# Kernel tuning notes

Measured on AMD Instinct MI355X. Metric: run time of the kernel, lower is better.

## Reference

```python
import jax, jax.numpy as jnp
import numpy as np

B, T, C = 1, 2048, 3072
H, HKV, D = 24, 8, 128          # heads, kv heads, head_dim
G = H // HKV                    # gqa groups = 3
ROPE_BASE = 10000.0


def _rope_cos_sin(seq_len, dim, dtype):
    inv_freq = 1.0 / (ROPE_BASE ** (jnp.arange(0, dim, 2, dtype=jnp.float32) / dim))
    t = jnp.arange(seq_len, dtype=jnp.float32)
    freqs = t[:, None] * inv_freq[None, :]            # [T, D/2]
    emb = jnp.concatenate([freqs, freqs], axis=-1)    # [T, D]
    return jnp.cos(emb).astype(dtype), jnp.sin(emb).astype(dtype)


def _rotate_half(x):
    h = x.shape[-1] // 2
    return jnp.concatenate([-x[..., h:], x[..., :h]], axis=-1)


def setup_inputs() -> dict:
    key = jax.random.key(0)
    ks = jax.random.split(key, 5)
    s = 0.02
    return {
        "x":  jax.random.normal(ks[0], (B, T, C), dtype=jnp.float32),
        "Wq": jax.random.normal(ks[1], (C, H * D), dtype=jnp.float32) * s,
        "Wk": jax.random.normal(ks[2], (C, HKV * D), dtype=jnp.float32) * s,
        "Wv": jax.random.normal(ks[3], (C, HKV * D), dtype=jnp.float32) * s,
        "Wo": jax.random.normal(ks[4], (C, C), dtype=jnp.float32) * s,
    }


def reference(x, Wq, Wk, Wv, Wo):
    b, t, c = x.shape
    # projections -> [B, H(or HKV), T, D]
    q = (x @ Wq).reshape(b, t, H, D).transpose(0, 2, 1, 3)
    k = (x @ Wk).reshape(b, t, HKV, D).transpose(0, 2, 1, 3)
    v = (x @ Wv).reshape(b, t, HKV, D).transpose(0, 2, 1, 3)
    # GQA: repeat_interleave kv heads to full head count
    k = jnp.repeat(k, G, axis=1)
    v = jnp.repeat(v, G, axis=1)
    # RoPE
    cos, sin = _rope_cos_sin(t, D, x.dtype)           # [T, D]
    cos = cos[None, None]                             # [1,1,T,D]
    sin = sin[None, None]
    q = q * cos + _rotate_half(q) * sin
    k = k * cos + _rotate_half(k) * sin
    # causal SDPA
    scale = 1.0 / jnp.sqrt(jnp.asarray(D, dtype=x.dtype))
    scores = jnp.einsum('bhqd,bhkd->bhqk', q, k) * scale
    causal = jnp.tril(jnp.ones((t, t), dtype=bool))
    scores = jnp.where(causal[None, None], scores, jnp.finfo(x.dtype).min)
    attn = jax.nn.softmax(scores, axis=-1)
    out = jnp.einsum('bhqk,bhkd->bhqd', attn, v)      # [B,H,T,D]
    out = out.transpose(0, 2, 1, 3).reshape(b, t, c)
    return out @ Wo
```

## Files before the change

kernel.cpp:

```cpp
#include <hip/hip_runtime.h>
#include <cstdint>

#define T_SEQ 2048
#define C_DIM 3072
#define NH    24
#define NKV   8
#define HD    128

typedef short  bf16x8 __attribute__((ext_vector_type(8)));
typedef float  f32x4  __attribute__((ext_vector_type(4)));

__device__ __forceinline__ ushort f2bf(float f) {
    union { float f; uint32_t u; } v; v.f = f;
    uint32_t r = (v.u + 0x7FFF + ((v.u >> 16) & 1)) >> 16;
    return (ushort)r;
}

__device__ __forceinline__ uint32_t cvtpk_bf16(float lo, float hi) {
    uint32_t r;
    asm("v_cvt_pk_bf16_f32 %0, %1, %2" : "=v"(r) : "v"(lo), "v"(hi));
    return r;
}

__device__ __forceinline__ float fast_exp2(float x) {
#if __has_builtin(__builtin_amdgcn_exp2f)
    return __builtin_amdgcn_exp2f(x);
#else
    return exp2f(x);
#endif
}

__device__ __forceinline__ void gll16(const void* g, void* lds) {
    __builtin_amdgcn_global_load_lds(
        (const __attribute__((address_space(1))) uint32_t*)g,
        (__attribute__((address_space(3))) uint32_t*)lds, 16, 0, 0);
}

__global__ __launch_bounds__(64) void rope_table(float* __restrict__ cosT,
                                                 float* __restrict__ sinT) {
    int t = blockIdx.x;
    int j = threadIdx.x;
    float inv = powf(10000.0f, -(float)j * (1.0f / 64.0f));
    float ang = (float)t * inv;
    cosT[t * 64 + j] = cosf(ang);
    sinT[t * 64 + j] = sinf(ang);
}

__global__ __launch_bounds__(256) void convert_x(const float* __restrict__ x,
                                                 ushort* __restrict__ xb) {
    int i = blockIdx.x * 256 + threadIdx.x;
    int stride = gridDim.x * 256;
    const int n4 = (T_SEQ * C_DIM) / 4;
    for (; i < n4; i += stride) {
        float4 v = ((const float4*)x)[i];
        ushort4 o;
        o.x = f2bf(v.x); o.y = f2bf(v.y); o.z = f2bf(v.z); o.w = f2bf(v.w);
        ((ushort4*)xb)[i] = o;
    }
}

__global__ __launch_bounds__(256) void transpose_w(const float* __restrict__ src,
                                                   ushort* __restrict__ dst,
                                                   int ldN) {
    __shared__ float sT[64][65];
    const int n0 = blockIdx.x * 64;
    const int k0 = blockIdx.y * 64;
    const int r  = threadIdx.x >> 4;
    const int c4 = (threadIdx.x & 15) * 4;
    #pragma unroll
    for (int i = 0; i < 4; ++i) {
        int kk = r + i * 16;
        float4 v = *(const float4*)&src[(size_t)(k0 + kk) * ldN + n0 + c4];
        sT[kk][c4 + 0] = v.x; sT[kk][c4 + 1] = v.y;
        sT[kk][c4 + 2] = v.z; sT[kk][c4 + 3] = v.w;
    }
    __syncthreads();
    #pragma unroll
    for (int i = 0; i < 4; ++i) {
        int nn = r + i * 16;
        ushort4 o;
        o.x = f2bf(sT[c4 + 0][nn]); o.y = f2bf(sT[c4 + 1][nn]);
        o.z = f2bf(sT[c4 + 2][nn]); o.w = f2bf(sT[c4 + 3][nn]);
        *(ushort4*)&dst[(size_t)(n0 + nn) * C_DIM + k0 + c4] = o;
    }
}

__global__ __launch_bounds__(256) void qkv_gemm_mfma(
    const ushort* __restrict__ xb, const ushort* __restrict__ WbT,
    const float* __restrict__ cosT, const float* __restrict__ sinT,
    ushort* __restrict__ Qb, ushort* __restrict__ Kb, ushort* __restrict__ Vt) {

    __shared__ ushort sA[128 * 64];
    __shared__ ushort sB[128 * 64];

    const int bx = blockIdx.x;
    const int by = blockIdx.y;
    const int tid = threadIdx.x;
    const int w = tid >> 6, l = tid & 63, g = l >> 4, c = l & 15;
    const int m0 = by * 128, n0 = bx * 128;

    f32x4 acc[2][8];
    #pragma unroll
    for (int m = 0; m < 2; ++m)
        #pragma unroll
        for (int n = 0; n < 8; ++n) acc[m][n] = {0.f, 0.f, 0.f, 0.f};

    const int ch = (w * 4) * 64 + l;
    for (int k0 = 0; k0 < C_DIM; k0 += 64) {
        __syncthreads();
        #pragma unroll
        for (int u = 0; u < 4; ++u) {
            int chu = ch + u * 64;
            int row = chu >> 3, sub = chu & 7;
            int sc  = sub ^ (row & 7);
            gll16(xb  + (size_t)(m0 + row) * C_DIM + k0 + sc * 8, &sA[(w * 4 + u) * 512]);
            gll16(WbT + (size_t)(n0 + row) * C_DIM + k0 + sc * 8, &sB[(w * 4 + u) * 512]);
        }
        __syncthreads();

        #pragma unroll
        for (int kc = 0; kc < 2; ++kc) {
            bf16x8 a[2], b[8];
            #pragma unroll
            for (int m = 0; m < 2; ++m) {
                int row = w * 32 + m * 16 + c;
                int chp = (kc * 4 + g) ^ (row & 7);
                a[m] = *(const bf16x8*)&sA[row * 64 + chp * 8];
            }
            #pragma unroll
            for (int n = 0; n < 8; ++n) {
                int row = n * 16 + c;
                int chp = (kc * 4 + g) ^ (row & 7);
                b[n] = *(const bf16x8*)&sB[row * 64 + chp * 8];
            }
            #pragma unroll
            for (int m = 0; m < 2; ++m)
                #pragma unroll
                for (int n = 0; n < 8; ++n)
                    acc[m][n] = __builtin_amdgcn_mfma_f32_16x16x32_bf16(a[m], b[n], acc[m][n], 0, 0, 0);
        }
    }

    if (bx < 32) {
        const bool isQ = (bx < 24);
        const float qscl = isQ ? (0.08838834764831845f * 1.4426950408889634f) : 1.0f;
        ushort* dst = isQ ? (Qb + (size_t)bx * T_SEQ * HD)
                          : (Kb + (size_t)(bx - 24) * T_SEQ * HD);
        #pragma unroll
        for (int m = 0; m < 2; ++m) {
            #pragma unroll
            for (int n = 0; n < 4; ++n) {
                #pragma unroll
                for (int r = 0; r < 4; ++r) {
                    int t = m0 + w * 32 + m * 16 + g * 4 + r;
                    int d = n * 16 + c;
                    float q1 = acc[m][n][r] * qscl, q2 = acc[m][n + 4][r] * qscl;
                    float cv = cosT[t * 64 + d], sv = sinT[t * 64 + d];
                    dst[(size_t)t * HD + d]      = f2bf(q1 * cv - q2 * sv);
                    dst[(size_t)t * HD + 64 + d] = f2bf(q2 * cv + q1 * sv);
                }
            }
        }
    } else {
        ushort* dst = Vt + (size_t)(bx - 32) * HD * T_SEQ;
        #pragma unroll
        for (int m = 0; m < 2; ++m) {
            #pragma unroll
            for (int n = 0; n < 8; ++n) {
                int d  = n * 16 + c;
                int t0 = m0 + w * 32 + m * 16 + g * 4;
                ushort4 pk;
                pk.x = f2bf(acc[m][n][0]); pk.y = f2bf(acc[m][n][1]);
                pk.z = f2bf(acc[m][n][2]); pk.w = f2bf(acc[m][n][3]);
                *(ushort4*)&dst[(size_t)d * T_SEQ + t0] = pk;
            }
        }
    }
}

__global__ __launch_bounds__(256) void attn_mfma(
    const ushort* __restrict__ Qb, const ushort* __restrict__ Kb,
    const ushort* __restrict__ Vt, ushort* __restrict__ AO) {

    __shared__ ushort sK[2][64 * 128];
    __shared__ ushort sV[2][128 * 64];
    __shared__ ushort sP[4][16][72];

    const int qt = (int)(gridDim.x - 1 - blockIdx.x);
    const int h  = blockIdx.y;
    const int kh = h / 3;
    const int tid = threadIdx.x;
    const int w = tid >> 6, l = tid & 63, g = l >> 4, c = l & 15;

    const ushort* Qp = Qb + (size_t)h  * T_SEQ * HD;
    const ushort* Kp = Kb + (size_t)kh * T_SEQ * HD;
    const ushort* Vp = Vt + (size_t)kh * HD * T_SEQ;

    const int myq = qt * 64 + w * 16 + c;
    bf16x8 qf[4];
    #pragma unroll
    for (int kc = 0; kc < 4; ++kc)
        qf[kc] = *(const bf16x8*)&Qp[(size_t)myq * HD + kc * 32 + g * 8];

    f32x4 o[8];
    #pragma unroll
    for (int n = 0; n < 8; ++n) o[n] = {0.f, 0.f, 0.f, 0.f};
    float m_run = -3.0e38f, l_run = 0.f;

    #define STAGE_KV(ktile, buf)                                                     \
        {                                                                            \
            _Pragma("unroll")                                                        \
            for (int u = 0; u < 4; ++u) {                                            \
                int chunk = (w * 4 + u) * 64 + l;                                    \
                int row = chunk >> 4;                                                \
                int sub = (chunk & 15) ^ (row & 7);                                  \
                gll16(Kp + (size_t)((ktile) * 64 + row) * HD + sub * 8,              \
                      &sK[buf][(w * 4 + u) * 512]);                                  \
            }                                                                        \
            _Pragma("unroll")                                                        \
            for (int u = 0; u < 4; ++u) {                                            \
                int chunk = (w * 4 + u) * 64 + l;                                    \
                int row = chunk >> 3;                                                \
                int sub = (chunk & 7) ^ (row & 7);                                   \
                gll16(Vp + (size_t)row * T_SEQ + (ktile) * 64 + sub * 8,             \
                      &sV[buf][(w * 4 + u) * 512]);                                  \
            }                                                                        \
        }

    int cur = 0;
    STAGE_KV(0, 0);
    __syncthreads();

    for (int kt = 0; kt <= qt; ++kt) {
        if (kt < qt) STAGE_KV(kt + 1, cur ^ 1);

        f32x4 sacc[4];
        #pragma unroll
        for (int nt = 0; nt < 4; ++nt) sacc[nt] = {0.f, 0.f, 0.f, 0.f};
        const ushort* sKc = &sK[cur][0];
        __builtin_amdgcn_s_setprio(1);
        #pragma unroll
        for (int nt = 0; nt < 4; ++nt) {
            int row = nt * 16 + c;
            #pragma unroll
            for (int kc = 0; kc < 4; ++kc) {
                int chp = (kc * 4 + g) ^ (row & 7);
                bf16x8 kf = *(const bf16x8*)&sKc[row * 128 + chp * 8];
                sacc[nt] = __builtin_amdgcn_mfma_f32_16x16x32_bf16(kf, qf[kc], sacc[nt], 0, 0, 0);
            }
        }
        __builtin_amdgcn_s_setprio(0);

        float p[16];
        float pm = -3.0e38f;
        #pragma unroll
        for (int nt = 0; nt < 4; ++nt) {
            #pragma unroll
            for (int r = 0; r < 4; ++r) {
                int key = kt * 64 + nt * 16 + g * 4 + r;
                float s = sacc[nt][r];
                s = (key > myq) ? -3.0e38f : s;
                p[nt * 4 + r] = s;
                pm = fmaxf(pm, s);
            }
        }
        pm = fmaxf(pm, __shfl_xor(pm, 16));
        pm = fmaxf(pm, __shfl_xor(pm, 32));

        if (!__all(pm <= m_run + 8.0f)) {
            float mnew = fmaxf(m_run, pm);
            float alpha = fast_exp2(m_run - mnew);
            m_run = mnew;
            l_run *= alpha;
            float aR[4];
            #pragma unroll
            for (int r = 0; r < 4; ++r) aR[r] = __shfl(alpha, g * 4 + r);
            #pragma unroll
            for (int n = 0; n < 8; ++n) {
                f32x4 t = o[n];
                t[0] *= aR[0]; t[1] *= aR[1]; t[2] *= aR[2]; t[3] *= aR[3];
                o[n] = t;
            }
        }
        float psum = 0.f;
        #pragma unroll
        for (int i = 0; i < 16; ++i) {
            float e = fast_exp2(p[i] - m_run);
            p[i] = e;
            psum += e;
        }
        psum += __shfl_xor(psum, 16);
        psum += __shfl_xor(psum, 32);
        l_run += psum;

        #pragma unroll
        for (int nt = 0; nt < 4; ++nt) {
            uint2 v;
            v.x = cvtpk_bf16(p[nt * 4 + 0], p[nt * 4 + 1]);
            v.y = cvtpk_bf16(p[nt * 4 + 2], p[nt * 4 + 3]);
            *(uint2*)&sP[w][c][nt * 16 + g * 4] = v;
        }

        const ushort* sVc = &sV[cur][0];
        __builtin_amdgcn_s_setprio(1);
        #pragma unroll
        for (int kc2 = 0; kc2 < 2; ++kc2) {
            bf16x8 pa = *(const bf16x8*)&sP[w][c][kc2 * 32 + g * 8];
            #pragma unroll
            for (int n = 0; n < 8; ++n) {
                int row = n * 16 + c;
                int chp = (kc2 * 4 + g) ^ (row & 7);
                bf16x8 vf = *(const bf16x8*)&sVc[row * 64 + chp * 8];
                o[n] = __builtin_amdgcn_mfma_f32_16x16x32_bf16(pa, vf, o[n], 0, 0, 0);
            }
        }
        __builtin_amdgcn_s_setprio(0);

        __syncthreads();
        cur ^= 1;
    }
    #undef STAGE_KV

    float invR[4];
    #pragma unroll
    for (int r = 0; r < 4; ++r) invR[r] = 1.0f / __shfl(l_run, g * 4 + r);
    #pragma unroll
    for (int n = 0; n < 8; ++n)
        #pragma unroll
        for (int r = 0; r < 4; ++r) {
            int t = qt * 64 + w * 16 + g * 4 + r;
            AO[(size_t)t * C_DIM + h * HD + n * 16 + c] = f2bf(o[n][r] * invR[r]);
        }
}

__global__ __launch_bounds__(256) void out_gemm_mfma(
    const ushort* __restrict__ Ab, const ushort* __restrict__ BT,
    float* __restrict__ outp) {

    __shared__ ushort sA[128 * 64];
    __shared__ ushort sB[128 * 64];

    const int bx = blockIdx.x;
    const int by = blockIdx.y;
    const int tid = threadIdx.x;
    const int w = tid >> 6, l = tid & 63, g = l >> 4, c = l & 15;
    const int m0 = by * 128, n0 = bx * 128;

    f32x4 acc[2][8];
    #pragma unroll
    for (int m = 0; m < 2; ++m)
        #pragma unroll
        for (int n = 0; n < 8; ++n) acc[m][n] = {0.f, 0.f, 0.f, 0.f};

    const int ch = (w * 4) * 64 + l;
    for (int k0 = 0; k0 < C_DIM; k0 += 64) {
        __syncthreads();
        #pragma unroll
        for (int u = 0; u < 4; ++u) {
            int chu = ch + u * 64;
            int row = chu >> 3, sub = chu & 7;
            int sc  = sub ^ (row & 7);
            gll16(Ab + (size_t)(m0 + row) * C_DIM + k0 + sc * 8, &sA[(w * 4 + u) * 512]);
            gll16(BT + (size_t)(n0 + row) * C_DIM + k0 + sc * 8, &sB[(w * 4 + u) * 512]);
        }
        __syncthreads();

        #pragma unroll
        for (int kc = 0; kc < 2; ++kc) {
            bf16x8 a[2], b[8];
            #pragma unroll
            for (int m = 0; m < 2; ++m) {
                int row = w * 32 + m * 16 + c;
                int chp = (kc * 4 + g) ^ (row & 7);
                a[m] = *(const bf16x8*)&sA[row * 64 + chp * 8];
            }
            #pragma unroll
            for (int n = 0; n < 8; ++n) {
                int row = n * 16 + c;
                int chp = (kc * 4 + g) ^ (row & 7);
                b[n] = *(const bf16x8*)&sB[row * 64 + chp * 8];
            }
            #pragma unroll
            for (int m = 0; m < 2; ++m)
                #pragma unroll
                for (int n = 0; n < 8; ++n)
                    acc[m][n] = __builtin_amdgcn_mfma_f32_16x16x32_bf16(a[m], b[n], acc[m][n], 0, 0, 0);
        }
    }

    #pragma unroll
    for (int m = 0; m < 2; ++m)
        #pragma unroll
        for (int n = 0; n < 8; ++n)
            #pragma unroll
            for (int r = 0; r < 4; ++r) {
                int t = m0 + w * 32 + m * 16 + g * 4 + r;
                outp[(size_t)t * C_DIM + n0 + n * 16 + c] = acc[m][n][r];
            }
}

extern "C" void kernel_launch(void* const* d_in, const int* in_sizes, int n_in,
                              void* d_out, int out_size, void* d_ws, size_t ws_size,
                              hipStream_t stream) {
    const float* x  = (const float*)d_in[0];
    const float* Wq = (const float*)d_in[1];
    const float* Wk = (const float*)d_in[2];
    const float* Wv = (const float*)d_in[3];
    const float* Wo = (const float*)d_in[4];

    char* ws = (char*)d_ws;
    float*  cosT = (float*)ws;                         ws += 2048 * 64 * 4;
    float*  sinT = (float*)ws;                         ws += 2048 * 64 * 4;
    ushort* WbT  = (ushort*)ws;                        ws += (size_t)5120 * 3072 * 2;
    ushort* WoT  = (ushort*)ws;                        ws += (size_t)3072 * 3072 * 2;
    ushort* Qb   = (ushort*)ws;                        ws += (size_t)NH  * T_SEQ * HD * 2;
    ushort* Kb   = (ushort*)ws;                        ws += (size_t)NKV * T_SEQ * HD * 2;
    ushort* Vt   = (ushort*)ws;                        ws += (size_t)NKV * T_SEQ * HD * 2;
    ushort* xb   = (ushort*)ws;
    ushort* AO   = xb;
    float*  out  = (float*)d_out;

    rope_table <<<dim3(2048),   dim3(64),  0, stream>>>(cosT, sinT);
    convert_x  <<<dim3(2048),   dim3(256), 0, stream>>>(x, xb);
    transpose_w<<<dim3(48, 48), dim3(256), 0, stream>>>(Wq, WbT,                       3072);
    transpose_w<<<dim3(16, 48), dim3(256), 0, stream>>>(Wk, WbT + (size_t)3072 * 3072, 1024);
    transpose_w<<<dim3(16, 48), dim3(256), 0, stream>>>(Wv, WbT + (size_t)4096 * 3072, 1024);
    transpose_w<<<dim3(48, 48), dim3(256), 0, stream>>>(Wo, WoT,                       3072);

    qkv_gemm_mfma<<<dim3(40, 16), dim3(256), 0, stream>>>(xb, WbT, cosT, sinT, Qb, Kb, Vt);
    attn_mfma    <<<dim3(32, 24), dim3(256), 0, stream>>>(Qb, Kb, Vt, AO);
    out_gemm_mfma<<<dim3(24, 16), dim3(256), 0, stream>>>(AO, WoT, out);
}
```

Before: 453.3 us.

## Use persistent atomic tile scheduler for attention and XCD-swizzle GEMM block mapping

The attention kernel becomes persistent: 512 workgroups repeatedly claim (query-tile, head) work items from a global atomic counter, heaviest causal tiles first, so the load balances dynamically instead of depending on hardware block dispatch order. The QKV and output GEMMs switch to a 1D grid with a block-index swizzle that groups neighbouring output tiles onto the same XCD to improve L2 reuse. This adds an extra zero-counter launch and an atomic plus a barrier per tile. The persistent loop may also raise register pressure.

```diff
diff --git a/kernel.cpp b/kernel.cpp
--- a/kernel.cpp
+++ b/kernel.cpp
@@ -6,6 +6,7 @@
 #define NH    24
 #define NKV   8
 #define HD    128
+#define N_TILES (32 * 24)
 
 typedef short  bf16x8 __attribute__((ext_vector_type(8)));
 typedef float  f32x4  __attribute__((ext_vector_type(4)));
@@ -35,6 +36,8 @@
         (const __attribute__((address_space(1))) uint32_t*)g,
         (__attribute__((address_space(3))) uint32_t*)lds, 16, 0, 0);
 }
+
+__global__ void zero_ctr(int* c) { *c = 0; }
 
 __global__ __launch_bounds__(64) void rope_table(float* __restrict__ cosT,
                                                  float* __restrict__ sinT) {
@@ -93,8 +96,10 @@
     __shared__ ushort sA[128 * 64];
     __shared__ ushort sB[128 * 64];
 
-    const int bx = blockIdx.x;
-    const int by = blockIdx.y;
+    const int bid = (int)blockIdx.x;
+    const int swzb = (bid & 7) * 80 + (bid >> 3);
+    const int bx = swzb % 40;
+    const int by = swzb / 40;
     const int tid = threadIdx.x;
     const int w = tid >> 6, l = tid & 63, g = l >> 4, c = l & 15;
     const int m0 = by * 128, n0 = bx * 128;
@@ -180,157 +185,166 @@
 
 __global__ __launch_bounds__(256) void attn_mfma(
     const ushort* __restrict__ Qb, const ushort* __restrict__ Kb,
-    const ushort* __restrict__ Vt, ushort* __restrict__ AO) {
+    const ushort* __restrict__ Vt, ushort* __restrict__ AO,
+    int* __restrict__ ctr) {
 
     __shared__ ushort sK[2][64 * 128];
     __shared__ ushort sV[2][128 * 64];
     __shared__ ushort sP[4][16][72];
-
-    const int qt = (int)(gridDim.x - 1 - blockIdx.x);
-    const int h  = blockIdx.y;
-    const int kh = h / 3;
+    __shared__ int s_tile;
+
     const int tid = threadIdx.x;
     const int w = tid >> 6, l = tid & 63, g = l >> 4, c = l & 15;
 
-    const ushort* Qp = Qb + (size_t)h  * T_SEQ * HD;
-    const ushort* Kp = Kb + (size_t)kh * T_SEQ * HD;
-    const ushort* Vp = Vt + (size_t)kh * HD * T_SEQ;
-
-    const int myq = qt * 64 + w * 16 + c;
-    bf16x8 qf[4];
-    #pragma unroll
-    for (int kc = 0; kc < 4; ++kc)
-        qf[kc] = *(const bf16x8*)&Qp[(size_t)myq * HD + kc * 32 + g * 8];
-
-    f32x4 o[8];
-    #pragma unroll
-    for (int n = 0; n < 8; ++n) o[n] = {0.f, 0.f, 0.f, 0.f};
-    float m_run = -3.0e38f, l_run = 0.f;
-
-    #define STAGE_KV(ktile, buf)                                                     \
-        {                                                                            \
-            _Pragma("unroll")                                                        \
-            for (int u = 0; u < 4; ++u) {                                            \
-                int chunk = (w * 4 + u) * 64 + l;                                    \
-                int row = chunk >> 4;                                                \
-                int sub = (chunk & 15) ^ (row & 7);                                  \
-                gll16(Kp + (size_t)((ktile) * 64 + row) * HD + sub * 8,              \
-                      &sK[buf][(w * 4 + u) * 512]);                                  \
-            }                                                                        \
-            _Pragma("unroll")                                                        \
-            for (int u = 0; u < 4; ++u) {                                            \
-                int chunk = (w * 4 + u) * 64 + l;                                    \
-                int row = chunk >> 3;                                                \
-                int sub = (chunk & 7) ^ (row & 7);                                   \
-                gll16(Vp + (size_t)row * T_SEQ + (ktile) * 64 + sub * 8,             \
-                      &sV[buf][(w * 4 + u) * 512]);                                  \
-            }                                                                        \
-        }
-
-    int cur = 0;
-    STAGE_KV(0, 0);
-    __syncthreads();
-
-    for (int kt = 0; kt <= qt; ++kt) {
-        if (kt < qt) STAGE_KV(kt + 1, cur ^ 1);
-
-        f32x4 sacc[4];
-        #pragma unroll
-        for (int nt = 0; nt < 4; ++nt) sacc[nt] = {0.f, 0.f, 0.f, 0.f};
-        const ushort* sKc = &sK[cur][0];
-        __builtin_amdgcn_s_setprio(1);
-        #pragma unroll
-        for (int nt = 0; nt < 4; ++nt) {
-            int row = nt * 16 + c;
-            #pragma unroll
-            for (int kc = 0; kc < 4; ++kc) {
-                int chp = (kc * 4 + g) ^ (row & 7);
-                bf16x8 kf = *(const bf16x8*)&sKc[row * 128 + chp * 8];
-                sacc[nt] = __builtin_amdgcn_mfma_f32_16x16x32_bf16(kf, qf[kc], sacc[nt], 0, 0, 0);
-            }
-        }
-        __builtin_amdgcn_s_setprio(0);
-
-        float p[16];
-        float pm = -3.0e38f;
-        #pragma unroll
-        for (int nt = 0; nt < 4; ++nt) {
+    for (;;) {
+        if (tid == 0) s_tile = atomicAdd(ctr, 1);
+        __syncthreads();
+        const int tau = s_tile;
+        if (tau >= N_TILES) break;
+        const int qt = 31 - tau / 24;
+        const int h  = tau % 24;
+        const int kh = h / 3;
+
+        const ushort* Qp = Qb + (size_t)h  * T_SEQ * HD;
+        const ushort* Kp = Kb + (size_t)kh * T_SEQ * HD;
+        const ushort* Vp = Vt + (size_t)kh * HD * T_SEQ;
+
+        const int myq = qt * 64 + w * 16 + c;
+        bf16x8 qf[4];
+        #pragma unroll
+        for (int kc = 0; kc < 4; ++kc)
+            qf[kc] = *(const bf16x8*)&Qp[(size_t)myq * HD + kc * 32 + g * 8];
+
+        f32x4 o[8];
+        #pragma unroll
+        for (int n = 0; n < 8; ++n) o[n] = {0.f, 0.f, 0.f, 0.f};
+        float m_run = -3.0e38f, l_run = 0.f;
+
+        #define STAGE_KV(ktile, buf)                                                 \
+            {                                                                        \
+                _Pragma("unroll")                                                    \
+                for (int u = 0; u < 4; ++u) {                                        \
+                    int chunk = (w * 4 + u) * 64 + l;                                \
+                    int row = chunk >> 4;                                            \
+                    int sub = (chunk & 15) ^ (row & 7);                              \
+                    gll16(Kp + (size_t)((ktile) * 64 + row) * HD + sub * 8,          \
+                          &sK[buf][(w * 4 + u) * 512]);                              \
+                }                                                                    \
+                _Pragma("unroll")                                                    \
+                for (int u = 0; u < 4; ++u) {                                        \
+                    int chunk = (w * 4 + u) * 64 + l;                                \
+                    int row = chunk >> 3;                                            \
+                    int sub = (chunk & 7) ^ (row & 7);                               \
+                    gll16(Vp + (size_t)row * T_SEQ + (ktile) * 64 + sub * 8,         \
+                          &sV[buf][(w * 4 + u) * 512]);                              \
+                }                                                                    \
+            }
+
+        int cur = 0;
+        STAGE_KV(0, 0);
+        __syncthreads();
+
+        for (int kt = 0; kt <= qt; ++kt) {
+            if (kt < qt) STAGE_KV(kt + 1, cur ^ 1);
+
+            f32x4 sacc[4];
+            #pragma unroll
+            for (int nt = 0; nt < 4; ++nt) sacc[nt] = {0.f, 0.f, 0.f, 0.f};
+            const ushort* sKc = &sK[cur][0];
+            __builtin_amdgcn_s_setprio(1);
+            #pragma unroll
+            for (int nt = 0; nt < 4; ++nt) {
+                int row = nt * 16 + c;
+                #pragma unroll
+                for (int kc = 0; kc < 4; ++kc) {
+                    int chp = (kc * 4 + g) ^ (row & 7);
+                    bf16x8 kf = *(const bf16x8*)&sKc[row * 128 + chp * 8];
+                    sacc[nt] = __builtin_amdgcn_mfma_f32_16x16x32_bf16(kf, qf[kc], sacc[nt], 0, 0, 0);
+                }
+            }
+            __builtin_amdgcn_s_setprio(0);
+
+            float p[16];
+            float pm = -3.0e38f;
+            #pragma unroll
+            for (int nt = 0; nt < 4; ++nt) {
+                #pragma unroll
+                for (int r = 0; r < 4; ++r) {
+                    int key = kt * 64 + nt * 16 + g * 4 + r;
+                    float s = sacc[nt][r];
+                    s = (key > myq) ? -3.0e38f : s;
+                    p[nt * 4 + r] = s;
+                    pm = fmaxf(pm, s);
+                }
+            }
+            pm = fmaxf(pm, __shfl_xor(pm, 16));
+            pm = fmaxf(pm, __shfl_xor(pm, 32));
+
+            if (!__all(pm <= m_run + 8.0f)) {
+                float mnew = fmaxf(m_run, pm);
+                float alpha = fast_exp2(m_run - mnew);
+                m_run = mnew;
+                l_run *= alpha;
+                float aR[4];
+                #pragma unroll
+                for (int r = 0; r < 4; ++r) aR[r] = __shfl(alpha, g * 4 + r);
+                #pragma unroll
+                for (int n = 0; n < 8; ++n) {
+                    f32x4 t = o[n];
+                    t[0] *= aR[0]; t[1] *= aR[1]; t[2] *= aR[2]; t[3] *= aR[3];
+                    o[n] = t;
+                }
+            }
+            float psum = 0.f;
+            #pragma unroll
+            for (int i = 0; i < 16; ++i) {
+                float e = fast_exp2(p[i] - m_run);
+                p[i] = e;
+                psum += e;
+            }
+            psum += __shfl_xor(psum, 16);
+            psum += __shfl_xor(psum, 32);
+            l_run += psum;
+
+            #pragma unroll
+            for (int nt = 0; nt < 4; ++nt) {
+                uint2 v;
+                v.x = cvtpk_bf16(p[nt * 4 + 0], p[nt * 4 + 1]);
+                v.y = cvtpk_bf16(p[nt * 4 + 2], p[nt * 4 + 3]);
+                *(uint2*)&sP[w][c][nt * 16 + g * 4] = v;
+            }
+
+            const ushort* sVc = &sV[cur][0];
+            __builtin_amdgcn_s_setprio(1);
+            #pragma unroll
+            for (int kc2 = 0; kc2 < 2; ++kc2) {
+                bf16x8 pa = *(const bf16x8*)&sP[w][c][kc2 * 32 + g * 8];
+                #pragma unroll
+                for (int n = 0; n < 8; ++n) {
+                    int row = n * 16 + c;
+                    int chp = (kc2 * 4 + g) ^ (row & 7);
+                    bf16x8 vf = *(const bf16x8*)&sVc[row * 64 + chp * 8];
+                    o[n] = __builtin_amdgcn_mfma_f32_16x16x32_bf16(pa, vf, o[n], 0, 0, 0);
+                }
+            }
+            __builtin_amdgcn_s_setprio(0);
+
+            __syncthreads();
+            cur ^= 1;
+        }
+        #undef STAGE_KV
+
+        float invR[4];
+        #pragma unroll
+        for (int r = 0; r < 4; ++r) invR[r] = 1.0f / __shfl(l_run, g * 4 + r);
+        #pragma unroll
+        for (int n = 0; n < 8; ++n)
             #pragma unroll
             for (int r = 0; r < 4; ++r) {
-                int key = kt * 64 + nt * 16 + g * 4 + r;
-                float s = sacc[nt][r];
-                s = (key > myq) ? -3.0e38f : s;
-                p[nt * 4 + r] = s;
-                pm = fmaxf(pm, s);
-            }
-        }
-        pm = fmaxf(pm, __shfl_xor(pm, 16));
-        pm = fmaxf(pm, __shfl_xor(pm, 32));
-
-        if (!__all(pm <= m_run + 8.0f)) {
-            float mnew = fmaxf(m_run, pm);
-            float alpha = fast_exp2(m_run - mnew);
-            m_run = mnew;
-            l_run *= alpha;
-            float aR[4];
-            #pragma unroll
-            for (int r = 0; r < 4; ++r) aR[r] = __shfl(alpha, g * 4 + r);
-            #pragma unroll
-            for (int n = 0; n < 8; ++n) {
-                f32x4 t = o[n];
-                t[0] *= aR[0]; t[1] *= aR[1]; t[2] *= aR[2]; t[3] *= aR[3];
-                o[n] = t;
-            }
-        }
-        float psum = 0.f;
-        #pragma unroll
-        for (int i = 0; i < 16; ++i) {
-            float e = fast_exp2(p[i] - m_run);
-            p[i] = e;
-            psum += e;
-        }
-        psum += __shfl_xor(psum, 16);
-        psum += __shfl_xor(psum, 32);
-        l_run += psum;
-
-        #pragma unroll
-        for (int nt = 0; nt < 4; ++nt) {
-            uint2 v;
-            v.x = cvtpk_bf16(p[nt * 4 + 0], p[nt * 4 + 1]);
-            v.y = cvtpk_bf16(p[nt * 4 + 2], p[nt * 4 + 3]);
-            *(uint2*)&sP[w][c][nt * 16 + g * 4] = v;
-        }
-
-        const ushort* sVc = &sV[cur][0];
-        __builtin_amdgcn_s_setprio(1);
-        #pragma unroll
-        for (int kc2 = 0; kc2 < 2; ++kc2) {
-            bf16x8 pa = *(const bf16x8*)&sP[w][c][kc2 * 32 + g * 8];
-            #pragma unroll
-            for (int n = 0; n < 8; ++n) {
-                int row = n * 16 + c;
-                int chp = (kc2 * 4 + g) ^ (row & 7);
-                bf16x8 vf = *(const bf16x8*)&sVc[row * 64 + chp * 8];
-                o[n] = __builtin_amdgcn_mfma_f32_16x16x32_bf16(pa, vf, o[n], 0, 0, 0);
-            }
-        }
-        __builtin_amdgcn_s_setprio(0);
-
-        __syncthreads();
-        cur ^= 1;
-    }
-    #undef STAGE_KV
-
-    float invR[4];
-    #pragma unroll
-    for (int r = 0; r < 4; ++r) invR[r] = 1.0f / __shfl(l_run, g * 4 + r);
-    #pragma unroll
-    for (int n = 0; n < 8; ++n)
-        #pragma unroll
-        for (int r = 0; r < 4; ++r) {
-            int t = qt * 64 + w * 16 + g * 4 + r;
-            AO[(size_t)t * C_DIM + h * HD + n * 16 + c] = f2bf(o[n][r] * invR[r]);
-        }
+                int t = qt * 64 + w * 16 + g * 4 + r;
+                AO[(size_t)t * C_DIM + h * HD + n * 16 + c] = f2bf(o[n][r] * invR[r]);
+            }
+    }
 }
 
 __global__ __launch_bounds__(256) void out_gemm_mfma(
@@ -340,8 +354,10 @@
     __shared__ ushort sA[128 * 64];
     __shared__ ushort sB[128 * 64];
 
-    const int bx = blockIdx.x;
-    const int by = blockIdx.y;
+    const int bid = (int)blockIdx.x;
+    const int swzb = (bid & 7) * 48 + (bid >> 3);
+    const int bx = swzb % 24;
+    const int by = swzb / 24;
     const int tid = threadIdx.x;
     const int w = tid >> 6, l = tid & 63, g = l >> 4, c = l & 15;
     const int m0 = by * 128, n0 = bx * 128;
@@ -409,6 +425,7 @@
     const float* Wo = (const float*)d_in[4];
 
     char* ws = (char*)d_ws;
+    int*    ctr  = (int*)ws;                           ws += 256;
     float*  cosT = (float*)ws;                         ws += 2048 * 64 * 4;
     float*  sinT = (float*)ws;                         ws += 2048 * 64 * 4;
     ushort* WbT  = (ushort*)ws;                        ws += (size_t)5120 * 3072 * 2;
@@ -420,6 +437,7 @@
     ushort* AO   = xb;
     float*  out  = (float*)d_out;
 
+    zero_ctr   <<<dim3(1),      dim3(1),   0, stream>>>(ctr);
     rope_table <<<dim3(2048),   dim3(64),  0, stream>>>(cosT, sinT);
     convert_x  <<<dim3(2048),   dim3(256), 0, stream>>>(x, xb);
     transpose_w<<<dim3(48, 48), dim3(256), 0, stream>>>(Wq, WbT,                       3072);
@@ -427,7 +445,7 @@
     transpose_w<<<dim3(16, 48), dim3(256), 0, stream>>>(Wv, WbT + (size_t)4096 * 3072, 1024);
     transpose_w<<<dim3(48, 48), dim3(256), 0, stream>>>(Wo, WoT,                       3072);
 
-    qkv_gemm_mfma<<<dim3(40, 16), dim3(256), 0, stream>>>(xb, WbT, cosT, sinT, Qb, Kb, Vt);
-    attn_mfma    <<<dim3(32, 24), dim3(256), 0, stream>>>(Qb, Kb, Vt, AO);
-    out_gemm_mfma<<<dim3(24, 16), dim3(256), 0, stream>>>(AO, WoT, out);
-}
+    qkv_gemm_mfma<<<dim3(640), dim3(256), 0, stream>>>(xb, WbT, cosT, sinT, Qb, Kb, Vt);
+    attn_mfma    <<<dim3(512), dim3(256), 0, stream>>>(Qb, Kb, Vt, AO, ctr);
+    out_gemm_mfma<<<dim3(384), dim3(256), 0, stream>>>(AO, WoT, out);
+}
```

After: 407.2 us. 1.11x faster.
